# Performance work log

Measured on AMD Instinct MI355X. Metric: run time of the kernel, lower is better.

Reference implementation:

```python
import jax, jax.numpy as jnp
import numpy as np

B, L, VOCAB = 32768, 512, 50000
CROP_RATIO, MIN_LEN = 0.8, 3
MASK_RATIO, MASK_TOKEN = 0.2, 0
REORDER_RATIO, MIN_W, MAX_W = 0.3, 2, 5


def setup_inputs() -> dict:
    key = jax.random.key(0)
    k1, k2 = jax.random.split(key)
    lens = jax.random.randint(k1, (B,), 1, L + 1)
    items = jax.random.randint(k2, (B, L), 1, VOCAB)
    pos = jnp.arange(L)[None, :]
    item_seq = jnp.where(pos < lens[:, None], items, 0).astype(jnp.int32)
    return {"item_seq": item_seq, "item_seq_len": lens.astype(jnp.int32)}


def _mask_aug(key, seq, lens):
    pos = jnp.arange(seq.shape[1])[None, :]
    valid = (pos < lens[:, None]) & (seq != 0)
    n_valid = valid.sum(axis=1)
    n_mask = jnp.minimum(jnp.maximum(1, (n_valid * MASK_RATIO).astype(jnp.int32)), n_valid)
    scores = jnp.where(valid, jax.random.uniform(key, seq.shape), jnp.inf)
    # rank of each position among valid positions by random score
    rank = jnp.argsort(jnp.argsort(scores, axis=1), axis=1)
    apply_row = (lens > 1) & (n_valid > 0)
    do_mask = valid & (rank < n_mask[:, None]) & apply_row[:, None]
    return jnp.where(do_mask, MASK_TOKEN, seq), lens


def _crop_aug(key, seq, lens):
    Lm = seq.shape[1]
    crop_len = jnp.minimum(jnp.maximum(MIN_LEN, (lens * CROP_RATIO).astype(jnp.int32)), lens)
    max_start = jnp.maximum(lens - crop_len + 1, 1)
    start = (jax.random.uniform(key, (seq.shape[0],)) * max_start).astype(jnp.int32)
    pos = jnp.arange(Lm)[None, :]
    idx = jnp.minimum(start[:, None] + pos, Lm - 1)
    cropped = jnp.where(pos < crop_len[:, None], jnp.take_along_axis(seq, idx, axis=1), 0)
    apply_row = lens > MIN_LEN
    return (jnp.where(apply_row[:, None], cropped, seq),
            jnp.where(apply_row, crop_len, lens))


def _reorder_aug(key, seq, lens):
    Bm, Lm = seq.shape
    k1, k2, k3, k4 = jax.random.split(key, 4)
    pos = jnp.arange(Lm)[None, :]
    valid = (pos < lens[:, None]) & (seq != 0)
    n_valid = valid.sum(axis=1)
    # valid positions first (in order), padding positions after
    valid_idx = jnp.argsort(jnp.where(valid, pos, Lm + pos), axis=1)
    max_w = jnp.minimum(n_valid, MAX_W)
    wsize = MIN_W + (jax.random.uniform(k1, (Bm,)) * jnp.maximum(max_w - MIN_W + 1, 1)).astype(jnp.int32)
    wsize = jnp.clip(wsize, MIN_W, MAX_W)
    max_start = jnp.maximum(n_valid - wsize + 1, 1)
    start = (jax.random.uniform(k2, (Bm,)) * max_start).astype(jnp.int32)
    apply_row = (lens > MIN_W) & (jax.random.uniform(k3, (Bm,)) <= REORDER_RATIO) & (n_valid >= MIN_W)
    k = jnp.arange(MAX_W)[None, :]
    slot_ok = k < wsize[:, None]
    win_cols = jnp.take_along_axis(valid_idx, jnp.minimum(start[:, None] + k, Lm - 1), axis=1)
    win_items = jnp.take_along_axis(seq, win_cols, axis=1)
    # random permutation within the (ragged) window via sorted random keys
    keys = jnp.where(slot_ok, jax.random.uniform(k4, (Bm, MAX_W)), jnp.inf)
    perm = jnp.argsort(keys, axis=1)
    shuffled = jnp.take_along_axis(win_items, perm, axis=1)
    vals = jnp.where(slot_ok & apply_row[:, None], shuffled, win_items)
    rows = jnp.arange(Bm)[:, None]
    return seq.at[rows, win_cols].set(vals), lens


def reference(item_seq, item_seq_len):
    key = jax.random.key(42)
    km, kc, kr = jax.random.split(key, 3)
    mask_seq, mask_len = _mask_aug(km, item_seq, item_seq_len)
    crop_seq, crop_len = _crop_aug(kc, item_seq, item_seq_len)
    reord_seq, reord_len = _reorder_aug(kr, item_seq, item_seq_len)
    return (mask_seq, mask_len, crop_seq, crop_len, reord_seq, reord_len)
```

## Files before the change

kernel.cpp:

```cpp
#include <hip/hip_runtime.h>
#include <stdint.h>


#define NB 32768
#define NL 512
#define NBL (NB * NL)

struct AugKeys {
  uint32_t km0, km1;
  uint32_t kc0, kc1;
  uint32_t r10, r11;
  uint32_t r20, r21;
  uint32_t r30, r31;
  uint32_t r40, r41;
};

__host__ __device__ __forceinline__ uint32_t rotl32(uint32_t x, uint32_t r) {
  return (x << r) | (x >> (32u - r));
}

__host__ __device__ inline void tf2x32(uint32_t k0, uint32_t k1,
                                       uint32_t x0, uint32_t x1,
                                       uint32_t& o0, uint32_t& o1) {
  const uint32_t ks2 = k0 ^ k1 ^ 0x1BD11BDAu;
#define TFR(r) { x0 += x1; x1 = rotl32(x1, r); x1 ^= x0; }
  x0 += k0; x1 += k1;
  TFR(13u) TFR(15u) TFR(26u) TFR(6u)
  x0 += k1; x1 += ks2 + 1u;
  TFR(17u) TFR(29u) TFR(16u) TFR(24u)
  x0 += ks2; x1 += k0 + 2u;
  TFR(13u) TFR(15u) TFR(26u) TFR(6u)
  x0 += k0; x1 += k1 + 3u;
  TFR(17u) TFR(29u) TFR(16u) TFR(24u)
  x0 += k1; x1 += ks2 + 4u;
  TFR(13u) TFR(15u) TFR(26u) TFR(6u)
  x0 += ks2; x1 += k0 + 5u;
#undef TFR
  o0 = x0; o1 = x1;
}

__device__ __forceinline__ float u01f(uint32_t bits) {
  return __uint_as_float((bits >> 9) | 0x3F800000u) - 1.0f;
}

__device__ __forceinline__ uint32_t rbits32(uint32_t k0, uint32_t k1, uint32_t i) {
  uint32_t o0, o1;
  tf2x32(k0, k1, 0u, i, o0, o1);
  return o0 ^ o1;
}

__global__ void __launch_bounds__(256)
aug_pipeline(const int* __restrict__ seq, const int* __restrict__ lens,
             int* __restrict__ out, AugKeys K)
{
  __shared__ int s_row[4][NL];
  __shared__ int s_hist[4][128];
  __shared__ int s_nbin[4];

  const int t = threadIdx.x;
  const int w = t >> 6;
  const int l = t & 63;
  const int b = blockIdx.x * 4 + w;
  const int len = __builtin_amdgcn_readfirstlane(lens[b]);
  const int* rowp = seq + (size_t)b * NL;

  int es[8];
#pragma unroll
  for (int it = 0; it < 8; ++it) es[it] = rowp[(it << 6) + l];

  s_hist[w][2 * l] = 0;
  s_hist[w][2 * l + 1] = 0;
  if (l == 0) s_nbin[w] = 0;

  float uval = 0.f;
  if (l < 9) {
    uint32_t kk0, kk1, f;
    if (l == 0)      { kk0 = K.kc0; kk1 = K.kc1; f = (uint32_t)b; }
    else if (l == 1) { kk0 = K.r10; kk1 = K.r11; f = (uint32_t)b; }
    else if (l == 2) { kk0 = K.r20; kk1 = K.r21; f = (uint32_t)b; }
    else if (l == 3) { kk0 = K.r30; kk1 = K.r31; f = (uint32_t)b; }
    else             { kk0 = K.r40; kk1 = K.r41; f = (uint32_t)b * 5u + (uint32_t)(l - 4); }
    uval = u01f(rbits32(kk0, kk1, f));
  }
  const float u_c = __shfl(uval, 0);
  const float u_w = __shfl(uval, 1);
  const float u_s = __shfl(uval, 2);
  const float u_a = __shfl(uval, 3);
  float u4[5];
#pragma unroll
  for (int k = 0; k < 5; ++k) u4[k] = __shfl(uval, 4 + k);

  uint32_t kk[8] = {0u, 0u, 0u, 0u, 0u, 0u, 0u, 0u};
  const uint32_t fbase = (uint32_t)b * NL;
#pragma unroll
  for (int p = 0; p < 4; ++p) {
    if ((p << 7) < len) {
      const int posA = (p << 7) + l;
      const int posB = (p << 7) + 64 + l;
      const uint32_t bitsA = rbits32(K.km0, K.km1, fbase + (uint32_t)posA);
      const uint32_t bitsB = rbits32(K.km0, K.km1, fbase + (uint32_t)posB);
      kk[2 * p]     = (bitsA & 0xFFFFFE00u) | (uint32_t)posA;
      kk[2 * p + 1] = (bitsB & 0xFFFFFE00u) | (uint32_t)posB;
    }
  }

  uint32_t vsm = 0;
  int nv = 0;
#pragma unroll
  for (int it = 0; it < 8; ++it) {
    const bool vs = ((it << 6) + l < len) && (es[it] != 0);
    vsm |= (uint32_t)vs << it;
    nv += (int)__popcll(__ballot(vs));
  }
  const int n_valid = __builtin_amdgcn_readfirstlane(nv);

#pragma unroll
  for (int it = 0; it < 8; ++it) s_row[w][(it << 6) + l] = es[it];

#pragma unroll
  for (int it = 0; it < 8; ++it) {
    if ((vsm >> it) & 1) atomicAdd(&s_hist[w][kk[it] >> 25], 1);
  }
  __builtin_amdgcn_wave_barrier();

  const int clen = min(max(3, (int)((float)len * 0.8f)), len);
  const int cms = max(len - clen + 1, 1);
  const int cstart = (int)(u_c * (float)cms);
  const bool apply_c = (len > 3);
  {
    int* cout = out + (size_t)NBL + NB + (size_t)b * NL;
#pragma unroll
    for (int it = 0; it < 8; ++it) {
      const int pos = (it << 6) + l;
      const int g = s_row[w][min(cstart + pos, NL - 1)];
      const int c = apply_c ? ((pos < clen) ? g : 0) : es[it];
      cout[pos] = c;
    }
  }

  if (l == 0) {
    out[(size_t)NBL + b] = len;
    out[2 * (size_t)NBL + NB + b] = apply_c ? clen : len;
    out[3 * (size_t)NBL + 2 * NB + b] = len;
  }

  {
    const int max_w = min(n_valid, 5);
    int wsize = 2 + (int)(u_w * (float)max(max_w - 1, 1));
    wsize = min(max(wsize, 2), 5);
    const int rms = max(n_valid - wsize + 1, 1);
    const int rstart = (int)(u_s * (float)rms);
    const bool apply_r = (len > 2) && (u_a <= 0.3f) && (n_valid >= 2);

    int cols[5], items[5];
    float fk[5];
#pragma unroll
    for (int k = 0; k < 5; ++k) {
      cols[k] = min(rstart + k, NL - 1);
      items[k] = s_row[w][cols[k]];
      fk[k] = (k < wsize) ? u4[k] : __int_as_float(0x7F800000);
    }
    int rank5[5];
#pragma unroll
    for (int k = 0; k < 5; ++k) {
      int rr = 0;
#pragma unroll
      for (int j = 0; j < 5; ++j) {
        rr += ((fk[j] < fk[k]) || (fk[j] == fk[k] && j < k)) ? 1 : 0;
      }
      rank5[k] = rr;
    }
    int valk[5];
#pragma unroll
    for (int p = 0; p < 5; ++p) {
      int sh = items[0];
#pragma unroll
      for (int k = 0; k < 5; ++k) if (rank5[k] == p) sh = items[k];
      valk[p] = (apply_r && p < wsize) ? sh : items[p];
    }

    int r8[8] = {es[0], es[1], es[2], es[3], es[4], es[5], es[6], es[7]};
#pragma unroll
    for (int k = 0; k < 5; ++k) {
      const int ck = cols[k];
#pragma unroll
      for (int it = 0; it < 8; ++it) {
        if ((ck >> 6) == it && (ck & 63) == l) r8[it] = valk[k];
      }
    }
    int* rout = out + 2 * (size_t)NBL + 2 * NB + (size_t)b * NL;
#pragma unroll
    for (int it = 0; it < 8; ++it) rout[(it << 6) + l] = r8[it];
  }

  const int h0 = s_hist[w][2 * l];
  const int h1 = s_hist[w][2 * l + 1];
  const int pair = h0 + h1;
  int incl = pair;
#pragma unroll
  for (int d = 1; d < 64; d <<= 1) {
    const int o = __shfl_up(incl, d);
    if (l >= d) incl += o;
  }
  const int ex0 = incl - pair;
  const int ex1 = ex0 + h0;
  const int n_mask = min(max(1, (int)((float)n_valid * 0.2f)), n_valid);
  const bool c0 = (h0 > 0) && (ex0 < n_mask) && (n_mask <= ex0 + h0);
  const bool c1 = (h1 > 0) && (ex1 < n_mask) && (n_mask <= ex1 + h1);
  const unsigned long long B0 = __ballot(c0);
  const unsigned long long B1 = __ballot(c1);
  int tbin = -1, below = 0;
  if (B0) {
    const int tl = __ffsll(B0) - 1;
    tbin = 2 * tl; below = __shfl(ex0, tl);
  } else if (B1) {
    const int tl = __ffsll(B1) - 1;
    tbin = 2 * tl + 1; below = __shfl(ex1, tl);
  }
  const int need = n_mask - below;

  uint32_t* s_bin = reinterpret_cast<uint32_t*>(s_row[w]);
#pragma unroll
  for (int it = 0; it < 8; ++it) {
    if (((vsm >> it) & 1) && (int)(kk[it] >> 25) == tbin) {
      s_bin[atomicAdd(&s_nbin[w], 1)] = kk[it];
    }
  }
  __builtin_amdgcn_wave_barrier();
  const int mtot = s_nbin[w];

  int rk[8] = {0, 0, 0, 0, 0, 0, 0, 0};
  for (int j = 0; j < mtot; ++j) {
    const uint32_t bk = s_bin[j];
#pragma unroll
    for (int it = 0; it < 8; ++it) rk[it] += (bk < kk[it]) ? 1 : 0;
  }

  const bool apply_m = (len > 1) && (n_valid > 0);
  int* mout = out + (size_t)b * NL;
#pragma unroll
  for (int it = 0; it < 8; ++it) {
    const int bin = (int)(kk[it] >> 25);
    const bool dm = apply_m && ((vsm >> it) & 1) &&
                    (bin < tbin || (bin == tbin && rk[it] < need));
    mout[(it << 6) + l] = dm ? 0 : es[it];
  }
}

extern "C" void kernel_launch(void* const* d_in, const int* in_sizes, int n_in,
                              void* d_out, int out_size, void* d_ws, size_t ws_size,
                              hipStream_t stream) {
  const int* seq  = (const int*)d_in[0];
  const int* lens = (const int*)d_in[1];
  int* out = (int*)d_out;

  AugKeys K;
  uint32_t kr0, kr1;
  tf2x32(0u, 42u, 0u, 0u, K.km0, K.km1);
  tf2x32(0u, 42u, 0u, 1u, K.kc0, K.kc1);
  tf2x32(0u, 42u, 0u, 2u, kr0, kr1);
  tf2x32(kr0, kr1, 0u, 0u, K.r10, K.r11);
  tf2x32(kr0, kr1, 0u, 1u, K.r20, K.r21);
  tf2x32(kr0, kr1, 0u, 2u, K.r30, K.r31);
  tf2x32(kr0, kr1, 0u, 3u, K.r40, K.r41);

  aug_pipeline<<<dim3(NB / 4), dim3(256), 0, stream>>>(seq, lens, out, K);
}
```

Before: 60.48 us.

## Split fused augmentation kernel into separate crop/reorder and mask kernels

Splits the single fused kernel into two launches. The first handles crop and reorder using a shared row copy, and the second handles the Threefry-based mask selection with its histogram and bin ranking. The aim is to lower register and LDS pressure in each kernel so more waves fit per CU and the PRNG-heavy mask path no longer stalls the streaming writes. In exchange, the input sequence is read from global memory twice and there is an extra launch.

```diff
diff --git a/kernel.cpp b/kernel.cpp
--- a/kernel.cpp
+++ b/kernel.cpp
@@ -50,12 +50,10 @@
 }
 
 __global__ void __launch_bounds__(256)
-aug_pipeline(const int* __restrict__ seq, const int* __restrict__ lens,
-             int* __restrict__ out, AugKeys K)
+aug_stream(const int* __restrict__ seq, const int* __restrict__ lens,
+           int* __restrict__ out, AugKeys K)
 {
   __shared__ int s_row[4][NL];
-  __shared__ int s_hist[4][128];
-  __shared__ int s_nbin[4];
 
   const int t = threadIdx.x;
   const int w = t >> 6;
@@ -67,10 +65,6 @@
   int es[8];
 #pragma unroll
   for (int it = 0; it < 8; ++it) es[it] = rowp[(it << 6) + l];
-
-  s_hist[w][2 * l] = 0;
-  s_hist[w][2 * l + 1] = 0;
-  if (l == 0) s_nbin[w] = 0;
 
   float uval = 0.f;
   if (l < 9) {
@@ -90,6 +84,109 @@
 #pragma unroll
   for (int k = 0; k < 5; ++k) u4[k] = __shfl(uval, 4 + k);
 
+#pragma unroll
+  for (int it = 0; it < 8; ++it) s_row[w][(it << 6) + l] = es[it];
+
+  int nv = 0;
+#pragma unroll
+  for (int it = 0; it < 8; ++it) {
+    nv += (int)__popcll(__ballot(((it << 6) + l < len) && (es[it] != 0)));
+  }
+  const int n_valid = __builtin_amdgcn_readfirstlane(nv);
+
+  __builtin_amdgcn_wave_barrier();
+
+  const int clen = min(max(3, (int)((float)len * 0.8f)), len);
+  const int cms = max(len - clen + 1, 1);
+  const int cstart = (int)(u_c * (float)cms);
+  const bool apply_c = (len > 3);
+  {
+    int* cout = out + (size_t)NBL + NB + (size_t)b * NL;
+#pragma unroll
+    for (int it = 0; it < 8; ++it) {
+      const int pos = (it << 6) + l;
+      const int g = s_row[w][min(cstart + pos, NL - 1)];
+      cout[pos] = apply_c ? ((pos < clen) ? g : 0) : es[it];
+    }
+  }
+
+  if (l == 0) {
+    out[(size_t)NBL + b] = len;
+    out[2 * (size_t)NBL + NB + b] = apply_c ? clen : len;
+    out[3 * (size_t)NBL + 2 * NB + b] = len;
+  }
+
+  const int max_w = min(n_valid, 5);
+  int wsize = 2 + (int)(u_w * (float)max(max_w - 1, 1));
+  wsize = min(max(wsize, 2), 5);
+  const int rms = max(n_valid - wsize + 1, 1);
+  const int rstart = (int)(u_s * (float)rms);
+  const bool apply_r = (len > 2) && (u_a <= 0.3f) && (n_valid >= 2);
+
+  int cols[5], items[5];
+  float fk[5];
+#pragma unroll
+  for (int k = 0; k < 5; ++k) {
+    cols[k] = min(rstart + k, NL - 1);
+    items[k] = s_row[w][cols[k]];
+    fk[k] = (k < wsize) ? u4[k] : __int_as_float(0x7F800000);
+  }
+  int rank5[5];
+#pragma unroll
+  for (int k = 0; k < 5; ++k) {
+    int rr = 0;
+#pragma unroll
+    for (int j = 0; j < 5; ++j) {
+      rr += ((fk[j] < fk[k]) || (fk[j] == fk[k] && j < k)) ? 1 : 0;
+    }
+    rank5[k] = rr;
+  }
+  int valk[5];
+#pragma unroll
+  for (int p = 0; p < 5; ++p) {
+    int sh = items[0];
+#pragma unroll
+    for (int k = 0; k < 5; ++k) if (rank5[k] == p) sh = items[k];
+    valk[p] = (apply_r && p < wsize) ? sh : items[p];
+  }
+
+  int r8[8] = {es[0], es[1], es[2], es[3], es[4], es[5], es[6], es[7]};
+#pragma unroll
+  for (int k = 0; k < 5; ++k) {
+    const int ck = cols[k];
+#pragma unroll
+    for (int it = 0; it < 8; ++it) {
+      if ((ck >> 6) == it && (ck & 63) == l) r8[it] = valk[k];
+    }
+  }
+  int* rout = out + 2 * (size_t)NBL + 2 * NB + (size_t)b * NL;
+#pragma unroll
+  for (int it = 0; it < 8; ++it) rout[(it << 6) + l] = r8[it];
+}
+
+__global__ void __launch_bounds__(256)
+aug_mask(const int* __restrict__ seq, const int* __restrict__ lens,
+         int* __restrict__ out, AugKeys K)
+{
+  __shared__ int s_hist[4][128];
+  __shared__ uint32_t s_bin[4][NL];
+  __shared__ int s_nbin[4];
+
+  const int t = threadIdx.x;
+  const int w = t >> 6;
+  const int l = t & 63;
+  const int b = blockIdx.x * 4 + w;
+  const int len = __builtin_amdgcn_readfirstlane(lens[b]);
+  const int* rowp = seq + (size_t)b * NL;
+
+  int es[8];
+#pragma unroll
+  for (int it = 0; it < 8; ++it) es[it] = rowp[(it << 6) + l];
+
+  s_hist[w][2 * l] = 0;
+  s_hist[w][2 * l + 1] = 0;
+  if (l == 0) s_nbin[w] = 0;
+
   uint32_t kk[8] = {0u, 0u, 0u, 0u, 0u, 0u, 0u, 0u};
   const uint32_t fbase = (uint32_t)b * NL;
 #pragma unroll
@@ -115,83 +212,10 @@
   const int n_valid = __builtin_amdgcn_readfirstlane(nv);
 
 #pragma unroll
-  for (int it = 0; it < 8; ++it) s_row[w][(it << 6) + l] = es[it];
-
-#pragma unroll
   for (int it = 0; it < 8; ++it) {
     if ((vsm >> it) & 1) atomicAdd(&s_hist[w][kk[it] >> 25], 1);
   }
   __builtin_amdgcn_wave_barrier();
-
-  const int clen = min(max(3, (int)((float)len * 0.8f)), len);
-  const int cms = max(len - clen + 1, 1);
-  const int cstart = (int)(u_c * (float)cms);
-  const bool apply_c = (len > 3);
-  {
-    int* cout = out + (size_t)NBL + NB + (size_t)b * NL;
-#pragma unroll
-    for (int it = 0; it < 8; ++it) {
-      const int pos = (it << 6) + l;
-      const int g = s_row[w][min(cstart + pos, NL - 1)];
-      const int c = apply_c ? ((pos < clen) ? g : 0) : es[it];
-      cout[pos] = c;
-    }
-  }
-
-  if (l == 0) {
-    out[(size_t)NBL + b] = len;
-    out[2 * (size_t)NBL + NB + b] = apply_c ? clen : len;
-    out[3 * (size_t)NBL + 2 * NB + b] = len;
-  }
-
-  {
-    const int max_w = min(n_valid, 5);
-    int wsize = 2 + (int)(u_w * (float)max(max_w - 1, 1));
-    wsize = min(max(wsize, 2), 5);
-    const int rms = max(n_valid - wsize + 1, 1);
-    const int rstart = (int)(u_s * (float)rms);
-    const bool apply_r = (len > 2) && (u_a <= 0.3f) && (n_valid >= 2);
-
-    int cols[5], items[5];
-    float fk[5];
-#pragma unroll
-    for (int k = 0; k < 5; ++k) {
-      cols[k] = min(rstart + k, NL - 1);
-      items[k] = s_row[w][cols[k]];
-      fk[k] = (k < wsize) ? u4[k] : __int_as_float(0x7F800000);
-    }
-    int rank5[5];
-#pragma unroll
-    for (int k = 0; k < 5; ++k) {
-      int rr = 0;
-#pragma unroll
-      for (int j = 0; j < 5; ++j) {
-        rr += ((fk[j] < fk[k]) || (fk[j] == fk[k] && j < k)) ? 1 : 0;
-      }
-      rank5[k] = rr;
-    }
-    int valk[5];
-#pragma unroll
-    for (int p = 0; p < 5; ++p) {
-      int sh = items[0];
-#pragma unroll
-      for (int k = 0; k < 5; ++k) if (rank5[k] == p) sh = items[k];
-      valk[p] = (apply_r && p < wsize) ? sh : items[p];
-    }
-
-    int r8[8] = {es[0], es[1], es[2], es[3], es[4], es[5], es[6], es[7]};
-#pragma unroll
-    for (int k = 0; k < 5; ++k) {
-      const int ck = cols[k];
-#pragma unroll
-      for (int it = 0; it < 8; ++it) {
-        if ((ck >> 6) == it && (ck & 63) == l) r8[it] = valk[k];
-      }
-    }
-    int* rout = out + 2 * (size_t)NBL + 2 * NB + (size_t)b * NL;
-#pragma unroll
-    for (int it = 0; it < 8; ++it) rout[(it << 6) + l] = r8[it];
-  }
 
   const int h0 = s_hist[w][2 * l];
   const int h1 = s_hist[w][2 * l + 1];
@@ -219,11 +243,10 @@
   }
   const int need = n_mask - below;
 
-  uint32_t* s_bin = reinterpret_cast<uint32_t*>(s_row[w]);
 #pragma unroll
   for (int it = 0; it < 8; ++it) {
     if (((vsm >> it) & 1) && (int)(kk[it] >> 25) == tbin) {
-      s_bin[atomicAdd(&s_nbin[w], 1)] = kk[it];
+      s_bin[w][atomicAdd(&s_nbin[w], 1)] = kk[it];
     }
   }
   __builtin_amdgcn_wave_barrier();
@@ -231,7 +254,7 @@
 
   int rk[8] = {0, 0, 0, 0, 0, 0, 0, 0};
   for (int j = 0; j < mtot; ++j) {
-    const uint32_t bk = s_bin[j];
+    const uint32_t bk = s_bin[w][j];
 #pragma unroll
     for (int it = 0; it < 8; ++it) rk[it] += (bk < kk[it]) ? 1 : 0;
   }
@@ -264,5 +287,6 @@
   tf2x32(kr0, kr1, 0u, 2u, K.r30, K.r31);
   tf2x32(kr0, kr1, 0u, 3u, K.r40, K.r41);
 
-  aug_pipeline<<<dim3(NB / 4), dim3(256), 0, stream>>>(seq, lens, out, K);
-}
+  aug_stream<<<dim3(NB / 4), dim3(256), 0, stream>>>(seq, lens, out, K);
+  aug_mask  <<<dim3(NB / 4), dim3(256), 0, stream>>>(seq, lens, out, K);
+}
```

After: 72.16 us. 19.3% more time.
